# Kernel optimization log

Hardware: AMD Instinct MI355X
Metric: run time of the kernel (lower is better)

The kernel has to match this reference:

```python
import jax, jax.numpy as jnp
import numpy as np
import math

QUERY_SIZE = 128
KEY_SIZE = 128
VALUE_SIZE = 64
ATTN_SIZE = 64
NQ = 4096
NK = 8192


def setup_inputs() -> dict:
    key = jax.random.key(0)
    ks = jax.random.split(key, 9)
    scale_q = 1.0 / math.sqrt(QUERY_SIZE)
    scale_k = 1.0 / math.sqrt(KEY_SIZE)
    scale_v = 1.0 / math.sqrt(VALUE_SIZE)
    return {
        "q": jax.random.normal(ks[0], (NQ, QUERY_SIZE), jnp.float32),
        "k": jax.random.normal(ks[1], (NK, KEY_SIZE), jnp.float32),
        "v": jax.random.normal(ks[2], (NK, VALUE_SIZE), jnp.float32),
        # nn.Linear weights: [out_features, in_features], y = x W^T + b
        "Wq": jax.random.uniform(ks[3], (ATTN_SIZE, QUERY_SIZE), jnp.float32, -scale_q, scale_q),
        "bq": jax.random.uniform(ks[4], (ATTN_SIZE,), jnp.float32, -scale_q, scale_q),
        "Wk": jax.random.uniform(ks[5], (ATTN_SIZE, KEY_SIZE), jnp.float32, -scale_k, scale_k),
        "bk": jax.random.uniform(ks[6], (ATTN_SIZE,), jnp.float32, -scale_k, scale_k),
        "Wv": jax.random.uniform(ks[7], (VALUE_SIZE, VALUE_SIZE), jnp.float32, -scale_v, scale_v),
        "bv": jax.random.uniform(ks[8], (VALUE_SIZE,), jnp.float32, -scale_v, scale_v),
    }


def reference(q, k, v, Wq, bq, Wk, bk, Wv, bv):
    # Linear projections (y = x W^T + b)
    query = q @ Wq.T + bq          # [Nq, A]
    key_p = k @ Wk.T + bk          # [Nk, A]
    value = v @ Wv.T + bv          # [Nk, Dv]
    # scaled dot-product scores
    g = (query @ key_p.T) / math.sqrt(ATTN_SIZE)   # [Nq, Nk]
    score = jax.nn.softmax(g, axis=-1)
    # sum(score[...,None] * value, axis=-2) == score @ value
    output = score @ value          # [Nq, Dv]
    return output
```

## Files before the change

### kernel.cpp

```cpp
#include <hip/hip_runtime.h>
#include <hip/hip_bf16.h>

typedef __bf16 bf16;
typedef __bf16 bf16x4 __attribute__((ext_vector_type(4)));
typedef __bf16 bf16x8 __attribute__((ext_vector_type(8)));
typedef float floatx4 __attribute__((ext_vector_type(4)));

#define MFMA16(A, B, C) __builtin_amdgcn_mfma_f32_16x16x32_bf16(A, B, C, 0, 0, 0)

constexpr int NQ = 4096;
constexpr int NK = 8192;
constexpr int AD = 64;
constexpr int KSPLIT = 16;
constexpr int BQ = 128;
constexpr int BK = 64;
constexpr int KPB = NK / KSPLIT;
constexpr int TILES = KPB / BK;
constexpr float QSCALE = 0.125f;

__device__ inline bf16x8 ld_cvt8(const float* __restrict__ p) {
  float4 a = *(const float4*)p;
  float4 b = *(const float4*)(p + 4);
  bf16x8 r = {(bf16)a.x, (bf16)a.y, (bf16)a.z, (bf16)a.w,
              (bf16)b.x, (bf16)b.y, (bf16)b.z, (bf16)b.w};
  return r;
}

__global__ __launch_bounds__(256) void proj_mfma(
    const float* __restrict__ q, const float* __restrict__ k,
    const float* __restrict__ v,
    const float* __restrict__ Wq, const float* __restrict__ bq,
    const float* __restrict__ Wk, const float* __restrict__ bk,
    const float* __restrict__ Wv, const float* __restrict__ bv,
    bf16* __restrict__ qout, bf16* __restrict__ kout, bf16* __restrict__ vtout) {
  const int tid = threadIdx.x;
  const int wave = tid >> 6, lane = tid & 63;
  const int l16 = lane & 15, quad = lane >> 4;
  const int b = blockIdx.x;

  if (b < 192) {
    const bool isQ = (b < 64);
    const float* X = isQ ? q : k;
    const float* W = isQ ? Wq : Wk;
    const float* bias = isQ ? bq : bk;
    bf16* Y = isQ ? qout : kout;
    const float oscale = isQ ? QSCALE : 1.0f;
    const int rowbase = (isQ ? b : b - 64) * 64 + wave * 16;

    bf16x8 bf_[4];
#pragma unroll
    for (int ks = 0; ks < 4; ++ks)
      bf_[ks] = ld_cvt8(X + (size_t)(rowbase + l16) * 128 + ks * 32 + quad * 8);
    bf16x8 af[4][4];
#pragma unroll
    for (int mt = 0; mt < 4; ++mt)
#pragma unroll
      for (int ks = 0; ks < 4; ++ks)
        af[mt][ks] = ld_cvt8(W + (size_t)(mt * 16 + l16) * 128 + ks * 32 + quad * 8);

    floatx4 acc[4];
#pragma unroll
    for (int mt = 0; mt < 4; ++mt) acc[mt] = (floatx4){0.f, 0.f, 0.f, 0.f};
#pragma unroll
    for (int mt = 0; mt < 4; ++mt)
#pragma unroll
      for (int ks = 0; ks < 4; ++ks)
        acc[mt] = MFMA16(af[mt][ks], bf_[ks], acc[mt]);

#pragma unroll
    for (int mt = 0; mt < 4; ++mt) {
      float4 bb = *(const float4*)(bias + mt * 16 + quad * 4);
      bf16x4 o = {(bf16)((acc[mt][0] + bb.x) * oscale),
                  (bf16)((acc[mt][1] + bb.y) * oscale),
                  (bf16)((acc[mt][2] + bb.z) * oscale),
                  (bf16)((acc[mt][3] + bb.w) * oscale)};
      *(bf16x4*)(Y + (size_t)(rowbase + l16) * 64 + mt * 16 + quad * 4) = o;
    }
  } else {
    const int keybase = (b - 192) * 64 + wave * 16;
    bf16x8 af2[2];
#pragma unroll
    for (int ks = 0; ks < 2; ++ks)
      af2[ks] = ld_cvt8(v + (size_t)(keybase + l16) * 64 + ks * 32 + quad * 8);
    bf16x8 bf2[4][2];
#pragma unroll
    for (int nt = 0; nt < 4; ++nt)
#pragma unroll
      for (int ks = 0; ks < 2; ++ks)
        bf2[nt][ks] = ld_cvt8(Wv + (size_t)(nt * 16 + l16) * 64 + ks * 32 + quad * 8);

    floatx4 acc[4];
#pragma unroll
    for (int nt = 0; nt < 4; ++nt) acc[nt] = (floatx4){0.f, 0.f, 0.f, 0.f};
#pragma unroll
    for (int nt = 0; nt < 4; ++nt)
#pragma unroll
      for (int ks = 0; ks < 2; ++ks)
        acc[nt] = MFMA16(af2[ks], bf2[nt][ks], acc[nt]);

#pragma unroll
    for (int nt = 0; nt < 4; ++nt) {
      float bvv = bv[nt * 16 + l16];
      bf16x4 o = {(bf16)(acc[nt][0] + bvv), (bf16)(acc[nt][1] + bvv),
                  (bf16)(acc[nt][2] + bvv), (bf16)(acc[nt][3] + bvv)};
      *(bf16x4*)(vtout + (size_t)(nt * 16 + l16) * NK + keybase + quad * 4) = o;
    }
  }
}

__global__ __launch_bounds__(256) void flash_kernel(
    const bf16* __restrict__ qp, const bf16* __restrict__ kp,
    const bf16* __restrict__ vt, bf16* __restrict__ Opart,
    float* __restrict__ lpart) {
  __shared__ __align__(16) bf16 Kt[BK][72];
  __shared__ __align__(16) bf16 Vts[AD][72];
  __shared__ __align__(16) bf16 Pt[4][32][72];

  const int tid = threadIdx.x;
  const int wave = tid >> 6;
  const int lane = tid & 63;
  const int l16 = lane & 15;
  const int quad = lane >> 4;
  const int ks = blockIdx.x;
  const int qb = blockIdx.y;
  const int qbase = qb * BQ + wave * 32;

  bf16x8 qf[2][2];
#pragma unroll
  for (int g = 0; g < 2; ++g)
#pragma unroll
    for (int c = 0; c < 2; ++c)
      qf[g][c] = *(const bf16x8*)(qp + (size_t)(qbase + g * 16 + l16) * AD +
                                  c * 32 + quad * 8);

  floatx4 o[2][4];
#pragma unroll
  for (int g = 0; g < 2; ++g)
#pragma unroll
    for (int nt = 0; nt < 4; ++nt)
      o[g][nt] = (floatx4){0.f, 0.f, 0.f, 0.f};
  float lsum[2] = {0.f, 0.f};

  for (int kt = 0; kt < TILES; ++kt) {
    const int keybase = ks * KPB + kt * BK;
    __syncthreads();
#pragma unroll
    for (int it = 0; it < 2; ++it) {
      int i = tid + it * 256;
      int row = i >> 3, cg = i & 7;
      *(bf16x8*)&Kt[row][cg * 8] =
          *(const bf16x8*)(kp + (size_t)(keybase + row) * AD + cg * 8);
      *(bf16x8*)&Vts[row][cg * 8] =
          *(const bf16x8*)(vt + (size_t)row * NK + keybase + cg * 8);
    }
    __syncthreads();

    floatx4 s[4][2];
#pragma unroll
    for (int st = 0; st < 4; ++st) {
      bf16x8 ka0 = *(const bf16x8*)&Kt[st * 16 + l16][quad * 8];
      bf16x8 ka1 = *(const bf16x8*)&Kt[st * 16 + l16][quad * 8 + 32];
#pragma unroll
      for (int g = 0; g < 2; ++g) {
        floatx4 acc = {0.f, 0.f, 0.f, 0.f};
        acc = MFMA16(ka0, qf[g][0], acc);
        acc = MFMA16(ka1, qf[g][1], acc);
        s[st][g] = acc;
      }
    }

#pragma unroll
    for (int st = 0; st < 4; ++st)
#pragma unroll
      for (int g = 0; g < 2; ++g) {
        float p0 = __expf(s[st][g][0]);
        float p1 = __expf(s[st][g][1]);
        float p2 = __expf(s[st][g][2]);
        float p3 = __expf(s[st][g][3]);
        lsum[g] += (p0 + p1) + (p2 + p3);
        bf16x4 pk = {(bf16)p0, (bf16)p1, (bf16)p2, (bf16)p3};
        *(bf16x4*)&Pt[wave][g * 16 + l16][st * 16 + quad * 4] = pk;
      }

    bf16x8 pf[2][2];
#pragma unroll
    for (int g = 0; g < 2; ++g)
#pragma unroll
      for (int c = 0; c < 2; ++c)
        pf[g][c] = *(const bf16x8*)&Pt[wave][g * 16 + l16][quad * 8 + c * 32];
#pragma unroll
    for (int nt = 0; nt < 4; ++nt) {
      bf16x8 vb0 = *(const bf16x8*)&Vts[nt * 16 + l16][quad * 8];
      bf16x8 vb1 = *(const bf16x8*)&Vts[nt * 16 + l16][quad * 8 + 32];
#pragma unroll
      for (int g = 0; g < 2; ++g) {
        o[g][nt] = MFMA16(pf[g][0], vb0, o[g][nt]);
        o[g][nt] = MFMA16(pf[g][1], vb1, o[g][nt]);
      }
    }
  }

#pragma unroll
  for (int g = 0; g < 2; ++g) {
    float t = lsum[g];
    t += __shfl_xor(t, 16, 64);
    t += __shfl_xor(t, 32, 64);
    lsum[g] = t;
  }

  bf16* ob = Opart + (size_t)ks * NQ * AD + (size_t)qbase * AD;
#pragma unroll
  for (int g = 0; g < 2; ++g)
#pragma unroll
    for (int nt = 0; nt < 4; ++nt)
#pragma unroll
      for (int r = 0; r < 4; ++r)
        ob[(size_t)(g * 16 + quad * 4 + r) * AD + nt * 16 + l16] =
            (bf16)o[g][nt][r];
  if (quad == 0) {
#pragma unroll
    for (int g = 0; g < 2; ++g)
      lpart[(size_t)ks * NQ + qbase + g * 16 + l16] = lsum[g];
  }
}

__global__ __launch_bounds__(256) void combine_kernel(
    const bf16* __restrict__ Opart, const float* __restrict__ lpart,
    float* __restrict__ out) {
  int t = blockIdx.x * 256 + threadIdx.x;
  int gid = t * 4;
  int qrow = gid >> 6;
  float ls = 0.f;
#pragma unroll
  for (int s = 0; s < KSPLIT; ++s) ls += lpart[(size_t)s * NQ + qrow];
  float a0 = 0.f, a1 = 0.f, a2 = 0.f, a3 = 0.f;
#pragma unroll
  for (int s = 0; s < KSPLIT; ++s) {
    bf16x4 ov = *(const bf16x4*)(Opart + (size_t)s * NQ * AD + gid);
    a0 += (float)ov[0];
    a1 += (float)ov[1];
    a2 += (float)ov[2];
    a3 += (float)ov[3];
  }
  float inv = 1.0f / ls;
  float4 res = {a0 * inv, a1 * inv, a2 * inv, a3 * inv};
  *(float4*)(out + gid) = res;
}

extern "C" void kernel_launch(void* const* d_in, const int* in_sizes, int n_in,
                              void* d_out, int out_size, void* d_ws,
                              size_t ws_size, hipStream_t stream) {
  const float* q = (const float*)d_in[0];
  const float* k = (const float*)d_in[1];
  const float* v = (const float*)d_in[2];
  const float* Wq = (const float*)d_in[3];
  const float* bq = (const float*)d_in[4];
  const float* Wk = (const float*)d_in[5];
  const float* bk = (const float*)d_in[6];
  const float* Wv = (const float*)d_in[7];
  const float* bv = (const float*)d_in[8];
  float* out = (float*)d_out;

  char* ws = (char*)d_ws;
  bf16* qout = (bf16*)(ws);
  bf16* kout = (bf16*)(ws + 524288);
  bf16* vtout = (bf16*)(ws + 1572864);
  bf16* Opart = (bf16*)(ws + 2621440);
  float* lpart = (float*)(ws + 2621440 + (size_t)KSPLIT * NQ * AD * 2);

  proj_mfma<<<320, 256, 0, stream>>>(q, k, v, Wq, bq, Wk, bk, Wv, bv, qout,
                                     kout, vtout);
  flash_kernel<<<dim3(KSPLIT, NQ / BQ), 256, 0, stream>>>(qout, kout, vtout,
                                                          Opart, lpart);
  combine_kernel<<<NQ * AD / 1024, 256, 0, stream>>>(Opart, lpart, out);
}
```

Measured before the change: 105.9 us.

## Load K/V fragments directly from global, drop LDS staging, use exp2

Removes the shared-memory staging of K and V tiles and the two block barriers per tile, so each wave reads its MFMA fragments straight from global memory (L2/L1). It doubles the key split to 32 for more blocks and sets launch bounds to request higher occupancy. It also folds log2(e) into the query scale so the softmax can use the hardware exp2 instruction directly. The trade-off is that each wave of a block re-reads the same K/V from cache, and the doubled split means more partial outputs to reduce.

```diff
diff --git a/kernel.cpp b/kernel.cpp
--- a/kernel.cpp
+++ b/kernel.cpp
@@ -11,12 +11,12 @@
 constexpr int NQ = 4096;
 constexpr int NK = 8192;
 constexpr int AD = 64;
-constexpr int KSPLIT = 16;
+constexpr int KSPLIT = 32;
 constexpr int BQ = 128;
 constexpr int BK = 64;
 constexpr int KPB = NK / KSPLIT;
 constexpr int TILES = KPB / BK;
-constexpr float QSCALE = 0.125f;
+constexpr float QSCALE = 0.125f * 1.4426950408889634f;
 
 __device__ inline bf16x8 ld_cvt8(const float* __restrict__ p) {
   float4 a = *(const float4*)p;
@@ -108,12 +108,10 @@
   }
 }
 
-__global__ __launch_bounds__(256) void flash_kernel(
+__global__ __launch_bounds__(256, 4) void flash_kernel(
     const bf16* __restrict__ qp, const bf16* __restrict__ kp,
     const bf16* __restrict__ vt, bf16* __restrict__ Opart,
     float* __restrict__ lpart) {
-  __shared__ __align__(16) bf16 Kt[BK][72];
-  __shared__ __align__(16) bf16 Vts[AD][72];
   __shared__ __align__(16) bf16 Pt[4][32][72];
 
   const int tid = threadIdx.x;
@@ -143,44 +141,26 @@
 
   for (int kt = 0; kt < TILES; ++kt) {
     const int keybase = ks * KPB + kt * BK;
-    __syncthreads();
-#pragma unroll
-    for (int it = 0; it < 2; ++it) {
-      int i = tid + it * 256;
-      int row = i >> 3, cg = i & 7;
-      *(bf16x8*)&Kt[row][cg * 8] =
-          *(const bf16x8*)(kp + (size_t)(keybase + row) * AD + cg * 8);
-      *(bf16x8*)&Vts[row][cg * 8] =
-          *(const bf16x8*)(vt + (size_t)row * NK + keybase + cg * 8);
-    }
-    __syncthreads();
-
-    floatx4 s[4][2];
+
 #pragma unroll
     for (int st = 0; st < 4; ++st) {
-      bf16x8 ka0 = *(const bf16x8*)&Kt[st * 16 + l16][quad * 8];
-      bf16x8 ka1 = *(const bf16x8*)&Kt[st * 16 + l16][quad * 8 + 32];
+      const bf16* krow = kp + (size_t)(keybase + st * 16 + l16) * AD + quad * 8;
+      bf16x8 ka0 = *(const bf16x8*)krow;
+      bf16x8 ka1 = *(const bf16x8*)(krow + 32);
 #pragma unroll
       for (int g = 0; g < 2; ++g) {
         floatx4 acc = {0.f, 0.f, 0.f, 0.f};
         acc = MFMA16(ka0, qf[g][0], acc);
         acc = MFMA16(ka1, qf[g][1], acc);
-        s[st][g] = acc;
-      }
-    }
-
-#pragma unroll
-    for (int st = 0; st < 4; ++st)
-#pragma unroll
-      for (int g = 0; g < 2; ++g) {
-        float p0 = __expf(s[st][g][0]);
-        float p1 = __expf(s[st][g][1]);
-        float p2 = __expf(s[st][g][2]);
-        float p3 = __expf(s[st][g][3]);
+        float p0 = __builtin_amdgcn_exp2f(acc[0]);
+        float p1 = __builtin_amdgcn_exp2f(acc[1]);
+        float p2 = __builtin_amdgcn_exp2f(acc[2]);
+        float p3 = __builtin_amdgcn_exp2f(acc[3]);
         lsum[g] += (p0 + p1) + (p2 + p3);
         bf16x4 pk = {(bf16)p0, (bf16)p1, (bf16)p2, (bf16)p3};
         *(bf16x4*)&Pt[wave][g * 16 + l16][st * 16 + quad * 4] = pk;
       }
+    }
 
     bf16x8 pf[2][2];
 #pragma unroll
@@ -188,10 +168,12 @@
 #pragma unroll
       for (int c = 0; c < 2; ++c)
         pf[g][c] = *(const bf16x8*)&Pt[wave][g * 16 + l16][quad * 8 + c * 32];
+
 #pragma unroll
     for (int nt = 0; nt < 4; ++nt) {
-      bf16x8 vb0 = *(const bf16x8*)&Vts[nt * 16 + l16][quad * 8];
-      bf16x8 vb1 = *(const bf16x8*)&Vts[nt * 16 + l16][quad * 8 + 32];
+      const bf16* vrow = vt + (size_t)(nt * 16 + l16) * NK + keybase + quad * 8;
+      bf16x8 vb0 = *(const bf16x8*)vrow;
+      bf16x8 vb1 = *(const bf16x8*)(vrow + 32);
 #pragma unroll
       for (int g = 0; g < 2; ++g) {
         o[g][nt] = MFMA16(pf[g][0], vb0, o[g][nt]);
```

Result: slower. 122.8 us (+16.0%).
